# Performance work log

Measured on AMD Instinct MI355X. Metric: run time of the kernel, lower is better.

Reference implementation:

```python
import jax, jax.numpy as jnp
import numpy as np

J = 29  # joints per frame (from fc = Linear(29*3, 2))
C = 3   # feature channels (GCNConv(3, 3))


def setup_inputs() -> dict:
    key = jax.random.key(0)
    ks = jax.random.split(key, 6)
    batch_size, num_frames = 256, 1024
    n_total = batch_size * num_frames * J
    x = jax.random.normal(ks[0], (n_total, C), dtype=jnp.float32)
    edge_index = jax.random.randint(ks[1], (2, 56), 0, J, dtype=jnp.int64)
    # GCNConv(3,3) params and fc Linear(87,2) params
    W = jax.random.normal(ks[2], (C, C), dtype=jnp.float32) / np.sqrt(C)
    b = jnp.zeros((C,), dtype=jnp.float32)
    fc_W = jax.random.normal(ks[3], (J * C, 2), dtype=jnp.float32) / np.sqrt(J * C)
    fc_b = jnp.zeros((2,), dtype=jnp.float32)
    return {"x": x, "edge_index": edge_index, "batch_size": batch_size,
            "num_frames": num_frames, "W": W, "b": b, "fc_W": fc_W, "fc_b": fc_b}


def reference(x, edge_index, batch_size, num_frames, W, b, fc_W, fc_b):
    num_joints = x.shape[0] // (batch_size * num_frames)  # == J
    F = batch_size * num_frames
    self_idx = jnp.arange(num_joints, dtype=edge_index.dtype)
    src = jnp.concatenate([edge_index[0], self_idx])  # add self loops (PyG default)
    dst = jnp.concatenate([edge_index[1], self_idx])
    # symmetric degree normalization D^{-1/2}(A+I)D^{-1/2}
    deg = jnp.zeros((num_joints,), x.dtype).at[dst].add(1.0)
    dinv = jnp.where(deg > 0, jax.lax.rsqrt(deg), 0.0)
    norm = dinv[src] * dinv[dst]  # [E+J]
    # transform then aggregate, vectorized over all frames at once
    xw = (x @ W).reshape(F, num_joints, -1)  # [F, J, C]
    msgs = xw[:, src, :] * norm[None, :, None]  # [F, E+J, C]
    agg = jnp.zeros_like(xw).at[:, dst, :].add(msgs) + b  # scatter-add to targets
    h = jax.nn.relu(agg).reshape(batch_size, num_frames, num_joints * W.shape[1])
    h = jnp.mean(h, axis=1)  # [B, J*C] mean over frames
    z = jax.nn.sigmoid(h @ fc_W + fc_b)  # [B, 2]
    return (h, z)
```

## Files before the change

kernel.cpp:

```cpp
#include <hip/hip_runtime.h>
#include <math.h>

#define J   29
#define CH  3
#define JC  87
#define E0  56
#define B   256
#define T   1024
#define FRAMES (B*T)
#define FPC 64
#define CPB 4
#define NBLK (FRAMES/(FPC*CPB))
#define CHUNK_FLOATS (FPC*JC)
#define CHUNK_BYTES (CHUNK_FLOATS*4)
#define BPB (T/(FPC*CPB))
#define SLOTS 4
#define PROWS 32
#define MAXOV 96
#define WAVES 8
#define RPW 4
#define NROUND 29

typedef const __attribute__((address_space(1))) void* gas_p;
typedef __attribute__((address_space(3))) void* las_p;

__global__ void prep_kernel(const int* __restrict__ ei,
                            int2* __restrict__ pairs,
                            int*  __restrict__ ov_rp,
                            int2* __restrict__ ov_pairs)
{
    __shared__ float M[J * J];
    __shared__ float dinv[J];
    __shared__ int   cnt_ov[J];
    int tid = threadIdx.x;

    for (int i = tid; i < J * J; i += 64) M[i] = 0.f;
    if (tid < J) {
        int d = 1;
        for (int e = 0; e < E0; ++e) d += (ei[E0 + e] == tid) ? 1 : 0;
        dinv[tid] = rsqrtf((float)d);
    }
    __syncthreads();

    if (tid < J) {
        for (int e = 0; e < E0; ++e) {
            if (ei[E0 + e] == tid) {
                int s = ei[e];
                M[tid * J + s] += dinv[s] * dinv[tid];
            }
        }
        M[tid * J + tid] += dinv[tid] * dinv[tid];
        int c = 0;
        for (int i = 0; i < J; ++i) c += (M[tid * J + i] != 0.f) ? 1 : 0;
        cnt_ov[tid] = (c > SLOTS) ? (c - SLOTS) : 0;
    }
    __syncthreads();

    if (tid == 0) {
        int a = 0;
        for (int j = 0; j < J; ++j) { ov_rp[j] = a; a += cnt_ov[j]; }
        for (int j = J; j <= 32; ++j) ov_rp[j] = a;
    }
    __syncthreads();

    if (tid < PROWS) {
        int2 zero; zero.x = 0; zero.y = 0;
        if (tid < J) {
            int s = 0, p = ov_rp[tid];
            for (int i = 0; i < J; ++i) {
                float v = M[tid * J + i];
                if (v != 0.f) {
                    if (s < SLOTS) {
                        int2 pr; pr.x = i * 16; pr.y = __float_as_int(v);
                        pairs[tid * SLOTS + s] = pr;
                    } else {
                        int2 pr; pr.x = (tid << 16) | (i * 16); pr.y = __float_as_int(v);
                        ov_pairs[p++] = pr;
                    }
                    ++s;
                }
            }
            for (; s < SLOTS; ++s) pairs[tid * SLOTS + s] = zero;
        } else {
            for (int s = 0; s < SLOTS; ++s) pairs[tid * SLOTS + s] = zero;
        }
    }
    __syncthreads();
    if (tid == 0) {
        int a = ov_rp[J];
        for (int i = a; i < MAXOV; ++i) { int2 pr; pr.x = 0; pr.y = 0; ov_pairs[i] = pr; }
    }
}

__launch_bounds__(512, 6)
__global__ void gcn_main(const float* __restrict__ x,
                         const float* __restrict__ Wp,
                         const float* __restrict__ bp,
                         const int2* __restrict__ pairs,
                         const int*  __restrict__ ov_rp,
                         const int2* __restrict__ ov_pairs,
                         float* __restrict__ partials) {
    __shared__ float4 xs4[FPC * J];

    int tid  = threadIdx.x;
    int lane = tid & 63;
    int wv   = tid >> 6;
    int rowbase = __builtin_amdgcn_readfirstlane(wv * RPW);

    float sW[9], sb[CH];
#pragma unroll
    for (int i = 0; i < 9; ++i) sW[i] = Wp[i];
#pragma unroll
    for (int i = 0; i < CH; ++i) sb[i] = bp[i];
    int ov0 = ov_rp[rowbase], ov1 = ov_rp[rowbase + RPW];

    const char* src = (const char*)(x + (size_t)blockIdx.x * (CPB * CHUNK_FLOATS));
    char* dst = (char*)xs4;
    const bool lastBlock = (blockIdx.x == NBLK - 1);

    float acc[RPW][CH];
#pragma unroll
    for (int r = 0; r < RPW; ++r)
#pragma unroll
        for (int c = 0; c < CH; ++c) acc[r][c] = 0.f;

    for (int c = 0; c < CPB; ++c) {
        __syncthreads();
        const char* s = src + (size_t)c * CHUNK_BYTES;
        const bool lastChunk = lastBlock && (c == CPB - 1);
        for (int r = wv; r < NROUND; r += WAVES) {
            int goff = r * 768 + lane * 12;
            if (lastChunk && r == NROUND - 1)
                goff = (goff > CHUNK_BYTES - 16) ? (CHUNK_BYTES - 16) : goff;
            __builtin_amdgcn_global_load_lds((gas_p)(s + goff),
                                             (las_p)(dst + r * 1024), 16, 0, 0);
        }
        asm volatile("s_waitcnt vmcnt(0)" ::: "memory");
        if (lastChunk && wv == (NROUND - 1) % WAVES && lane == 0) {
            volatile float* slot = (volatile float*)(xs4 + (FPC * J - 1));
            float a = slot[1], b2 = slot[2], c2 = slot[3];
            slot[0] = a; slot[1] = b2; slot[2] = c2;
        }
        __syncthreads();

        const char* xf = (const char*)xs4 + lane * (J * 16);

        float y[RPW][CH];
#pragma unroll
        for (int R = 0; R < RPW; ++R) {
            float a0 = 0.f, a1 = 0.f, a2 = 0.f;
#pragma unroll
            for (int sl = 0; sl < SLOTS; ++sl) {
                int2 pr = pairs[(rowbase + R) * SLOTS + sl];
                float v = __int_as_float(pr.y);
                float4 q = *(const float4*)(xf + pr.x);
                a0 += v * q.x;
                a1 += v * q.y;
                a2 += v * q.z;
            }
            y[R][0] = a0; y[R][1] = a1; y[R][2] = a2;
        }

        for (int e = ov0; e < ov1; ++e) {
            int2 pr = ov_pairs[e];
            int row = pr.x >> 16;
            int off = pr.x & 0xFFFF;
            float v = __int_as_float(pr.y);
            float4 q = *(const float4*)(xf + off);
            float d0 = v * q.x, d1 = v * q.y, d2 = v * q.z;
#pragma unroll
            for (int R = 0; R < RPW; ++R) {
                if (row == rowbase + R) {
                    y[R][0] += d0; y[R][1] += d1; y[R][2] += d2;
                }
            }
        }

#pragma unroll
        for (int R = 0; R < RPW; ++R)
#pragma unroll
            for (int ch = 0; ch < CH; ++ch) {
                float t = y[R][0] * sW[0 * CH + ch]
                        + y[R][1] * sW[1 * CH + ch]
                        + y[R][2] * sW[2 * CH + ch]
                        + sb[ch];
                acc[R][ch] += fmaxf(t, 0.f);
            }
    }

#pragma unroll
    for (int R = 0; R < RPW; ++R)
#pragma unroll
        for (int ch = 0; ch < CH; ++ch) {
            float v = acc[R][ch];
#pragma unroll
            for (int m = 1; m < 64; m <<= 1) v += __shfl_xor(v, m, 64);
            acc[R][ch] = v;
        }
    if (lane == 0) {
#pragma unroll
        for (int R = 0; R < RPW; ++R) {
            int j = rowbase + R;
            if (j < J) {
#pragma unroll
                for (int ch = 0; ch < CH; ++ch)
                    partials[(size_t)blockIdx.x * JC + j * CH + ch] = acc[R][ch];
            }
        }
    }
}

__global__ void finalize_kernel(const float* __restrict__ partials,
                                const float* __restrict__ fcW,
                                const float* __restrict__ fcb,
                                float* __restrict__ out) {
    __shared__ float h[JC];
    int b = blockIdx.x, tid = threadIdx.x;
    if (tid < JC) {
        float a = 0.f;
#pragma unroll
        for (int p = 0; p < BPB; ++p)
            a += partials[(size_t)(b * BPB + p) * JC + tid];
        a *= (1.0f / (float)T);
        h[tid] = a;
        out[(size_t)b * JC + tid] = a;
    }
    __syncthreads();
    if (tid < 2) {
        float a = fcb[tid];
        for (int r = 0; r < JC; ++r) a += h[r] * fcW[r * 2 + tid];
        out[(size_t)B * JC + b * 2 + tid] = 1.0f / (1.0f + expf(-a));
    }
}

extern "C" void kernel_launch(void* const* d_in, const int* in_sizes, int n_in,
                              void* d_out, int out_size, void* d_ws, size_t ws_size,
                              hipStream_t stream) {
    const float* x   = (const float*)d_in[0];
    const int*   ei  = (const int*)d_in[1];
    const float* W   = (const float*)d_in[4];
    const float* bb  = (const float*)d_in[5];
    const float* fcW = (const float*)d_in[6];
    const float* fcb = (const float*)d_in[7];

    char* ws = (char*)d_ws;
    int2* pairs    = (int2*)ws;
    int2* ov_pairs = pairs + PROWS * SLOTS;
    int*  ov_rp    = (int*)(ov_pairs + MAXOV);
    float* partials = (float*)(ws + 4096);

    prep_kernel<<<1, 64, 0, stream>>>(ei, pairs, ov_rp, ov_pairs);
    gcn_main<<<NBLK, WAVES * 64, 0, stream>>>(x, W, bb, pairs, ov_rp, ov_pairs, partials);
    finalize_kernel<<<B, 128, 0, stream>>>(partials, fcW, fcb, (float*)d_out);
}
```

Baseline: 44.07 us.

## Double-buffer LDS chunk staging and cache edge pairs in registers and LDS

Adds a second LDS buffer so the asynchronous global-to-LDS load of the next chunk overlaps computation on the current one, using partial vmcnt waits and raw barriers. It doubles chunks per block, which halves the grid, and lowers the occupancy hint. It also preloads the per-row edge pairs into registers and the overflow pairs into LDS, avoiding repeated global loads inside the loop. This costs more LDS and registers per block, and the hand-tuned vmcnt counts depend on how loads are distributed per wave.

```diff
diff --git a/kernel.cpp b/kernel.cpp
--- a/kernel.cpp
+++ b/kernel.cpp
@@ -9,7 +9,7 @@
 #define T   1024
 #define FRAMES (B*T)
 #define FPC 64
-#define CPB 4
+#define CPB 8
 #define NBLK (FRAMES/(FPC*CPB))
 #define CHUNK_FLOATS (FPC*JC)
 #define CHUNK_BYTES (CHUNK_FLOATS*4)
@@ -92,7 +92,19 @@
     }
 }
 
-__launch_bounds__(512, 6)
+__device__ __forceinline__ void stage_chunk(const char* __restrict__ s,
+                                            char* d, int lane, int wv,
+                                            bool lastChunk) {
+    for (int r = wv; r < NROUND; r += WAVES) {
+        int goff = r * 768 + lane * 12;
+        if (lastChunk && r == NROUND - 1)
+            goff = (goff > CHUNK_BYTES - 16) ? (CHUNK_BYTES - 16) : goff;
+        __builtin_amdgcn_global_load_lds((gas_p)(s + goff),
+                                         (las_p)(d + r * 1024), 16, 0, 0);
+    }
+}
+
+__launch_bounds__(512, 4)
 __global__ void gcn_main(const float* __restrict__ x,
                          const float* __restrict__ Wp,
                          const float* __restrict__ bp,
@@ -100,7 +112,8 @@
                          const int*  __restrict__ ov_rp,
                          const int2* __restrict__ ov_pairs,
                          float* __restrict__ partials) {
-    __shared__ float4 xs4[FPC * J];
+    __shared__ float4 xs4[2][FPC * J];
+    __shared__ int2   s_ovp[MAXOV];
 
     int tid  = threadIdx.x;
     int lane = tid & 63;
@@ -113,9 +126,16 @@
 #pragma unroll
     for (int i = 0; i < CH; ++i) sb[i] = bp[i];
     int ov0 = ov_rp[rowbase], ov1 = ov_rp[rowbase + RPW];
+    int2 pr_[RPW][SLOTS];
+#pragma unroll
+    for (int R = 0; R < RPW; ++R)
+#pragma unroll
+        for (int sl = 0; sl < SLOTS; ++sl)
+            pr_[R][sl] = pairs[(rowbase + R) * SLOTS + sl];
+    if (tid < MAXOV) s_ovp[tid] = ov_pairs[tid];
+    __syncthreads();
 
     const char* src = (const char*)(x + (size_t)blockIdx.x * (CPB * CHUNK_FLOATS));
-    char* dst = (char*)xs4;
     const bool lastBlock = (blockIdx.x == NBLK - 1);
 
     float acc[RPW][CH];
@@ -124,26 +144,38 @@
 #pragma unroll
         for (int c = 0; c < CH; ++c) acc[r][c] = 0.f;
 
+    stage_chunk(src, (char*)xs4[0], lane, wv, false);
+
     for (int c = 0; c < CPB; ++c) {
-        __syncthreads();
-        const char* s = src + (size_t)c * CHUNK_BYTES;
+        float4* bufc = xs4[c & 1];
         const bool lastChunk = lastBlock && (c == CPB - 1);
-        for (int r = wv; r < NROUND; r += WAVES) {
-            int goff = r * 768 + lane * 12;
-            if (lastChunk && r == NROUND - 1)
-                goff = (goff > CHUNK_BYTES - 16) ? (CHUNK_BYTES - 16) : goff;
-            __builtin_amdgcn_global_load_lds((gas_p)(s + goff),
-                                             (las_p)(dst + r * 1024), 16, 0, 0);
-        }
-        asm volatile("s_waitcnt vmcnt(0)" ::: "memory");
-        if (lastChunk && wv == (NROUND - 1) % WAVES && lane == 0) {
-            volatile float* slot = (volatile float*)(xs4 + (FPC * J - 1));
+
+        asm volatile("" ::: "memory");
+        __builtin_amdgcn_s_barrier();
+        asm volatile("" ::: "memory");
+
+        if (c + 1 < CPB) {
+            stage_chunk(src + (size_t)(c + 1) * CHUNK_BYTES,
+                        (char*)xs4[(c + 1) & 1], lane, wv,
+                        lastBlock && (c + 1 == CPB - 1));
+            if (wv < 5) asm volatile("s_waitcnt vmcnt(4)" ::: "memory");
+            else        asm volatile("s_waitcnt vmcnt(3)" ::: "memory");
+        } else {
+            asm volatile("s_waitcnt vmcnt(0)" ::: "memory");
+        }
+
+        if (lastChunk && wv == 4 && lane == 0) {
+            volatile float* slot = (volatile float*)(bufc + (FPC * J - 1));
             float a = slot[1], b2 = slot[2], c2 = slot[3];
             slot[0] = a; slot[1] = b2; slot[2] = c2;
-        }
-        __syncthreads();
-
-        const char* xf = (const char*)xs4 + lane * (J * 16);
+            asm volatile("s_waitcnt lgkmcnt(0)" ::: "memory");
+        }
+
+        asm volatile("" ::: "memory");
+        __builtin_amdgcn_s_barrier();
+        __builtin_amdgcn_sched_barrier(0);
+
+        const char* xf = (const char*)bufc + lane * (J * 16);
 
         float y[RPW][CH];
 #pragma unroll
@@ -151,7 +183,7 @@
             float a0 = 0.f, a1 = 0.f, a2 = 0.f;
 #pragma unroll
             for (int sl = 0; sl < SLOTS; ++sl) {
-                int2 pr = pairs[(rowbase + R) * SLOTS + sl];
+                int2 pr = pr_[R][sl];
                 float v = __int_as_float(pr.y);
                 float4 q = *(const float4*)(xf + pr.x);
                 a0 += v * q.x;
@@ -162,7 +194,7 @@
         }
 
         for (int e = ov0; e < ov1; ++e) {
-            int2 pr = ov_pairs[e];
+            int2 pr = s_ovp[e];
             int row = pr.x >> 16;
             int off = pr.x & 0xFFFF;
             float v = __int_as_float(pr.y);
```

New measurement: 42.55 us. 3.5% less time.
